# Kernel optimization log

Hardware: AMD Instinct MI355X
Metric: run time of the kernel (lower is better)

Reference implementation:

```python
import jax, jax.numpy as jnp
import numpy as np

NU, NM, E, L = 100000, 20000, 3200000, 1000000
FD, H = 128, 64


def setup_inputs() -> dict:
    key = jax.random.key(0)
    ks = jax.random.split(key, 32)
    s = 0.05
    inp = {
        'movie_x': jax.random.normal(ks[0], (NM, FD), jnp.float32),
        'edge_src_user': jax.random.randint(ks[1], (E,), 0, NU),
        'edge_dst_movie': jax.random.randint(ks[2], (E,), 0, NM),
        'label_user': jax.random.randint(ks[3], (L,), 0, NU),
        'label_movie': jax.random.randint(ks[4], (L,), 0, NM),
        'user_emb': jax.random.normal(ks[5], (NU, H), jnp.float32) * s,
        'proj_w': jax.random.normal(ks[6], (FD, H), jnp.float32) * s,
        'proj_b': jnp.zeros((H,), jnp.float32),
        'dec_w1': jax.random.normal(ks[7], (2 * H, H), jnp.float32) * s,
        'dec_b1': jnp.zeros((H,), jnp.float32),
        'dec_w2': jax.random.normal(ks[8], (H, 1), jnp.float32) * s,
        'dec_b2': jnp.zeros((1,), jnp.float32),
    }
    i = 9
    for layer in ('1', '2'):
        for rel in ('um', 'mu'):
            inp[f'w{layer}_{rel}_l'] = jax.random.normal(ks[i], (H, H), jnp.float32) * s; i += 1
            inp[f'b{layer}_{rel}_l'] = jnp.zeros((H,), jnp.float32)
            inp[f'w{layer}_{rel}_r'] = jax.random.normal(ks[i], (H, H), jnp.float32) * s; i += 1
    return inp


def _sage(x_src, x_dst, e_src, e_dst, n_dst, w_l, b_l, w_r):
    # PyG SAGEConv, aggr='mean': out = lin_l(mean_j x_src[j]) + lin_r(x_dst)
    msg = x_src[e_src]                                      # [E, H] gather
    agg = jax.ops.segment_sum(msg, e_dst, num_segments=n_dst)
    cnt = jax.ops.segment_sum(jnp.ones((e_dst.shape[0],), x_src.dtype), e_dst, num_segments=n_dst)
    agg = agg / jnp.maximum(cnt, 1.0)[:, None]
    return agg @ w_l + b_l + x_dst @ w_r


def reference(movie_x, edge_src_user, edge_dst_movie, label_user, label_movie,
              user_emb, proj_w, proj_b,
              w1_um_l, b1_um_l, w1_um_r, w1_mu_l, b1_mu_l, w1_mu_r,
              w2_um_l, b2_um_l, w2_um_r, w2_mu_l, b2_mu_l, w2_mu_r,
              dec_w1, dec_b1, dec_w2, dec_b2):
    nu, nm = user_emb.shape[0], movie_x.shape[0]
    user0 = user_emb
    movie0 = movie_x @ proj_w + proj_b
    # conv1 (user->movie and movie->user), then ReLU
    movie1 = jax.nn.relu(_sage(user0, movie0, edge_src_user, edge_dst_movie, nm, w1_um_l, b1_um_l, w1_um_r))
    user1 = jax.nn.relu(_sage(movie0, user0, edge_dst_movie, edge_src_user, nu, w1_mu_l, b1_mu_l, w1_mu_r))
    # conv2 (no activation)
    movie2 = _sage(user1, movie1, edge_src_user, edge_dst_movie, nm, w2_um_l, b2_um_l, w2_um_r)
    user2 = _sage(movie1, user1, edge_dst_movie, edge_src_user, nu, w2_mu_l, b2_mu_l, w2_mu_r)
    # edge decoder: gather -> concat -> MLP
    x = jnp.concatenate([user2[label_user], movie2[label_movie]], axis=-1)  # [L, 2H]
    x = jax.nn.relu(x @ dec_w1 + dec_b1)
    return x @ dec_w2 + dec_b2
```

## Files before the change

### kernel.cpp

```cpp
#include <hip/hip_runtime.h>

static constexpr int NU = 100000;
static constexpr int NM = 20000;
static constexpr int NE = 3200000;
static constexpr int NL = 1000000;
static constexpr int FD = 128;
static constexpr int H  = 64;

static constexpr int MBK = 16;
static constexpr int UBK = 64;
static constexpr int NBM = NM / MBK;
static constexpr int NBU = (NU + UBK - 1) / UBK;
static constexpr int NBT = NBM + NBU;
static constexpr int BIN_CHUNK = 16384;
static constexpr int CAP_M = 4096;
static constexpr int CAP_U = 3072;

typedef __attribute__((ext_vector_type(8))) short short8v;
typedef __attribute__((ext_vector_type(4))) float f32x4;

__device__ __forceinline__ ushort bf16rne(float x) {
  unsigned u = __float_as_uint(x);
  return (ushort)((u + 0x7fffu + ((u >> 16) & 1u)) >> 16);
}

__global__ void k_binit2(int* __restrict__ bcur_m, int* __restrict__ bcur_u) {
  int i = blockIdx.x * 256 + threadIdx.x;
  if (i < NBM) bcur_m[i] = i * CAP_M;
  if (i < NBU) bcur_u[i] = i * CAP_U;
}

__global__ void __launch_bounds__(256) k_bin(const int* __restrict__ esrc,
                                             const int* __restrict__ edst,
                                             int* __restrict__ bcur_m,
                                             int* __restrict__ bcur_u,
                                             unsigned* __restrict__ pairs_m,
                                             unsigned* __restrict__ pairs_u) {
  __shared__ int cnt[NBT];
  __shared__ int base[NBT];
  int tid = threadIdx.x;
  for (int i = tid; i < NBT; i += 256) cnt[i] = 0;
  __syncthreads();
  int e0 = blockIdx.x * BIN_CHUNK;
  int e1 = min(e0 + BIN_CHUNK, NE);
  for (int e = e0 + tid; e < e1; e += 256) {
    int s = esrc[e], d = edst[e];
    atomicAdd(&cnt[d >> 4], 1);
    atomicAdd(&cnt[NBM + (s >> 6)], 1);
  }
  __syncthreads();
  for (int i = tid; i < NBT; i += 256) {
    int c = cnt[i];
    if (c > 0)
      base[i] = (i < NBM) ? atomicAdd(&bcur_m[i], c) : atomicAdd(&bcur_u[i - NBM], c);
    cnt[i] = 0;
  }
  __syncthreads();
  for (int e = e0 + tid; e < e1; e += 256) {
    int s = esrc[e], d = edst[e];
    int bm = d >> 4;
    int r = atomicAdd(&cnt[bm], 1);
    pairs_m[base[bm] + r] = ((unsigned)(d & 15) << 17) | (unsigned)s;
    int bu = NBM + (s >> 6);
    int r2 = atomicAdd(&cnt[bu], 1);
    pairs_u[base[bu] + r2] = ((unsigned)(s & 63) << 15) | (unsigned)d;
  }
}

template <int NPB>
__global__ void __launch_bounds__(256) k_sortb3(const unsigned* __restrict__ pairs,
                                                const int* __restrict__ bcur,
                                                int* __restrict__ start,
                                                int* __restrict__ deg,
                                                int* __restrict__ out_idx,
                                                int n, int shift, unsigned mask, int cap) {
  __shared__ int cnt[NPB];
  __shared__ int cbase[NPB];
  int tid = threadIdx.x;
  if (tid < NPB) cnt[tid] = 0;
  __syncthreads();
  int e0 = blockIdx.x * cap;
  int e1 = bcur[blockIdx.x];
  for (int e = e0 + tid; e < e1; e += 256) {
    unsigned v = pairs[e];
    atomicAdd(&cnt[v >> shift], 1);
  }
  __syncthreads();
  if (tid < 64) {
    int c = (tid < NPB) ? cnt[tid] : 0;
    int v = c;
    #pragma unroll
    for (int off = 1; off < NPB; off <<= 1) {
      int t = __shfl_up(v, off, 64);
      if (tid >= off) v += t;
    }
    if (tid < NPB) {
      int node = blockIdx.x * NPB + tid;
      int basee = e0 + v - c;
      cbase[tid] = basee;
      if (node < n) { start[node] = basee; deg[node] = c; }
      cnt[tid] = 0;
    }
  }
  __syncthreads();
  for (int e = e0 + tid; e < e1; e += 256) {
    unsigned v = pairs[e];
    int loc = (int)(v >> shift);
    int r = atomicAdd(&cnt[loc], 1);
    out_idx[cbase[loc] + r] = (int)(v & mask);
  }
}

__global__ void __launch_bounds__(256) k_agg2c(
    int gm,
    const ushort* __restrict__ fM, const int* __restrict__ stM, const int* __restrict__ dgM,
    const int* __restrict__ idxM, float* __restrict__ outM, int nM,
    const ushort* __restrict__ fU, const int* __restrict__ stU, const int* __restrict__ dgU,
    const int* __restrict__ idxU, float* __restrict__ outU, int nU) {
  const ushort* feat; const int* st; const int* dg; const int* idxs; float* out; int n, b;
  if ((int)blockIdx.x < gm) { feat = fM; st = stM; dg = dgM; idxs = idxM; out = outM; n = nM; b = blockIdx.x; }
  else { feat = fU; st = stU; dg = dgU; idxs = idxU; out = outU; n = nU; b = blockIdx.x - gm; }
  int lane = threadIdx.x & 63;
  int f4 = lane & 15, p = lane >> 4;
  int d = b * 4 + (threadIdx.x >> 6);
  if (d >= n) return;
  int s = st[d], degn = dg[d];
  int e = s + degn;
  float a0 = 0.f, a1 = 0.f, a2 = 0.f, a3 = 0.f;
  int i = s;
  for (; i + 16 <= e; i += 16) {
    int s0 = idxs[i + 0 + p];
    int s1 = idxs[i + 4 + p];
    int s2 = idxs[i + 8 + p];
    int s3 = idxs[i + 12 + p];
    uint2 v0 = *(const uint2*)(feat + ((size_t)s0 << 6) + (f4 << 2));
    uint2 v1 = *(const uint2*)(feat + ((size_t)s1 << 6) + (f4 << 2));
    uint2 v2 = *(const uint2*)(feat + ((size_t)s2 << 6) + (f4 << 2));
    uint2 v3 = *(const uint2*)(feat + ((size_t)s3 << 6) + (f4 << 2));
    a0 += __uint_as_float(v0.x << 16); a1 += __uint_as_float(v0.x & 0xffff0000u);
    a2 += __uint_as_float(v0.y << 16); a3 += __uint_as_float(v0.y & 0xffff0000u);
    a0 += __uint_as_float(v1.x << 16); a1 += __uint_as_float(v1.x & 0xffff0000u);
    a2 += __uint_as_float(v1.y << 16); a3 += __uint_as_float(v1.y & 0xffff0000u);
    a0 += __uint_as_float(v2.x << 16); a1 += __uint_as_float(v2.x & 0xffff0000u);
    a2 += __uint_as_float(v2.y << 16); a3 += __uint_as_float(v2.y & 0xffff0000u);
    a0 += __uint_as_float(v3.x << 16); a1 += __uint_as_float(v3.x & 0xffff0000u);
    a2 += __uint_as_float(v3.y << 16); a3 += __uint_as_float(v3.y & 0xffff0000u);
  }
  for (; i < e; i += 4) {
    int ii = i + p;
    bool ok = ii < e;
    int sj = idxs[ok ? ii : i];
    uint2 v = *(const uint2*)(feat + ((size_t)sj << 6) + (f4 << 2));
    if (!ok) { v.x = 0u; v.y = 0u; }
    a0 += __uint_as_float(v.x << 16); a1 += __uint_as_float(v.x & 0xffff0000u);
    a2 += __uint_as_float(v.y << 16); a3 += __uint_as_float(v.y & 0xffff0000u);
  }
  a0 += __shfl_xor(a0, 16, 64); a1 += __shfl_xor(a1, 16, 64);
  a2 += __shfl_xor(a2, 16, 64); a3 += __shfl_xor(a3, 16, 64);
  a0 += __shfl_xor(a0, 32, 64); a1 += __shfl_xor(a1, 32, 64);
  a2 += __shfl_xor(a2, 32, 64); a3 += __shfl_xor(a3, 32, 64);
  if (p == 0) {
    float inv = 1.f / fmaxf((float)degn, 1.f);
    float4 o = make_float4(a0 * inv, a1 * inv, a2 * inv, a3 * inv);
    *(float4*)&out[((size_t)d << 6) + (f4 << 2)] = o;
  }
}

__global__ void __launch_bounds__(256) k_proj16(const float* __restrict__ x,
                                                const float* __restrict__ w,
                                                const float* __restrict__ b,
                                                float* __restrict__ out,
                                                ushort* __restrict__ outh) {
  __shared__ float sw[FD * H];
  __shared__ float sx[16][FD];
  int tid = threadIdx.x;
  int r0 = blockIdx.x * 16;
  #pragma unroll
  for (int it = 0; it < 8; ++it) {
    int idx = tid + it * 256;
    ((float4*)sw)[idx] = ((const float4*)w)[idx];
  }
  #pragma unroll
  for (int it = 0; it < 2; ++it) {
    int idx = tid + it * 256;
    int row = idx >> 5, q = idx & 31;
    *(float4*)&sx[row][q * 4] = ((const float4*)x)[(size_t)(r0 + row) * 32 + q];
  }
  __syncthreads();
  int col = tid & 63, rg = tid >> 6;
  float bb = b[col];
  float acc[4];
  #pragma unroll
  for (int j = 0; j < 4; ++j) acc[j] = bb;
  #pragma unroll 4
  for (int k4 = 0; k4 < 32; ++k4) {
    float w0 = sw[(k4 * 4 + 0) * H + col], w1 = sw[(k4 * 4 + 1) * H + col];
    float w2 = sw[(k4 * 4 + 2) * H + col], w3 = sw[(k4 * 4 + 3) * H + col];
    #pragma unroll
    for (int j = 0; j < 4; ++j) {
      float4 a = *(const float4*)&sx[rg + j * 4][k4 * 4];
      acc[j] += a.x * w0 + a.y * w1 + a.z * w2 + a.w * w3;
    }
  }
  #pragma unroll
  for (int j = 0; j < 4; ++j) {
    size_t o = (size_t)(r0 + rg + j * 4) * H + col;
    out[o] = acc[j];
    outh[o] = bf16rne(acc[j]);
  }
}

__global__ void __launch_bounds__(256) k_sage16(
    int gm,
    const float* __restrict__ aggM, const float* __restrict__ xdM,
    const float* __restrict__ wlM, const float* __restrict__ wrM,
    const float* __restrict__ blM, float* __restrict__ outfM, ushort* __restrict__ outhM,
    const float* __restrict__ aggU, const float* __restrict__ xdU,
    const float* __restrict__ wlU, const float* __restrict__ wrU,
    const float* __restrict__ blU, float* __restrict__ outfU, ushort* __restrict__ outhU,
    int relu) {
  __shared__ float swl[H * H];
  __shared__ float swr[H * H];
  __shared__ float sa[16][H];
  __shared__ float sd[16][H];
  int tid = threadIdx.x;
  const float *agg, *xd, *wl, *wr, *bl; float* outf; ushort* outh; int r0;
  if ((int)blockIdx.x < gm) {
    agg = aggM; xd = xdM; wl = wlM; wr = wrM; bl = blM; outf = outfM; outh = outhM;
    r0 = blockIdx.x * 16;
  } else {
    agg = aggU; xd = xdU; wl = wlU; wr = wrU; bl = blU; outf = outfU; outh = outhU;
    r0 = (blockIdx.x - gm) * 16;
  }
  #pragma unroll
  for (int it = 0; it < 4; ++it) {
    int idx = tid + it * 256;
    ((float4*)swl)[idx] = ((const float4*)wl)[idx];
    ((float4*)swr)[idx] = ((const float4*)wr)[idx];
  }
  {
    int row = tid >> 4, q = tid & 15;
    *(float4*)&sa[row][q * 4] = ((const float4*)agg)[(size_t)(r0 + row) * 16 + q];
    *(float4*)&sd[row][q * 4] = ((const float4*)xd)[(size_t)(r0 + row) * 16 + q];
  }
  __syncthreads();
  int col = tid & 63, rg = tid >> 6;
  float b = bl[col];
  float acc[4];
  #pragma unroll
  for (int j = 0; j < 4; ++j) acc[j] = b;
  #pragma unroll 4
  for (int k4 = 0; k4 < 16; ++k4) {
    float w0 = swl[(k4 * 4 + 0) * H + col], w1 = swl[(k4 * 4 + 1) * H + col];
    float w2 = swl[(k4 * 4 + 2) * H + col], w3 = swl[(k4 * 4 + 3) * H + col];
    float v0 = swr[(k4 * 4 + 0) * H + col], v1 = swr[(k4 * 4 + 1) * H + col];
    float v2 = swr[(k4 * 4 + 2) * H + col], v3 = swr[(k4 * 4 + 3) * H + col];
    #pragma unroll
    for (int j = 0; j < 4; ++j) {
      int r = rg + j * 4;
      float4 a = *(const float4*)&sa[r][k4 * 4];
      float4 d = *(const float4*)&sd[r][k4 * 4];
      acc[j] += a.x * w0 + a.y * w1 + a.z * w2 + a.w * w3;
      acc[j] += d.x * v0 + d.y * v1 + d.z * v2 + d.w * v3;
    }
  }
  #pragma unroll
  for (int j = 0; j < 4; ++j) {
    int r = rg + j * 4;
    float v = relu ? fmaxf(acc[j], 0.f) : acc[j];
    size_t o = (size_t)(r0 + r) * H + col;
    if (outf) outf[o] = v;
    if (outh) outh[o] = bf16rne(v);
  }
}

__global__ void __launch_bounds__(256) k_cvtb(const float* __restrict__ src,
                                              ushort* __restrict__ dst, int n4) {
  int i = blockIdx.x * 256 + threadIdx.x;
  if (i >= n4) return;
  float4 v = ((const float4*)src)[i];
  ushort4 o;
  o.x = bf16rne(v.x); o.y = bf16rne(v.y); o.z = bf16rne(v.z); o.w = bf16rne(v.w);
  ((ushort4*)dst)[i] = o;
}

__global__ void k_packw(const float* __restrict__ w1, ushort* __restrict__ pw) {
  int tid = threadIdx.x;
  for (int it = 0; it < 4; ++it) {
    int q = tid + it * 256;
    int kt = q >> 8, ct = (q >> 6) & 3, l = q & 63;
    int kg = l >> 4, cg = l & 15;
    #pragma unroll
    for (int j = 0; j < 8; ++j) {
      int k = kt * 32 + kg * 8 + j;
      int c = ct * 16 + cg;
      float x = w1[k * 64 + c];
      unsigned u = __float_as_uint(x);
      unsigned r = (u + 0x7fffu + ((u >> 16) & 1u)) >> 16;
      float res = x - __uint_as_float(r << 16);
      pw[q * 8 + j] = (ushort)r;
      pw[8192 + q * 8 + j] = (ushort)(__float_as_uint(res) >> 16);
    }
  }
}

__global__ void __launch_bounds__(256) k_dec_mfma(
    const ushort* __restrict__ uhi, const ushort* __restrict__ mhi,
    const int* __restrict__ lu, const int* __restrict__ lm,
    const ushort* __restrict__ pw,
    const float* __restrict__ b1, const float* __restrict__ w2,
    const float* __restrict__ b2, float* __restrict__ out) {
  __shared__ ushort sB[2 * 16 * 64 * 8];
  int tid = threadIdx.x;
  #pragma unroll
  for (int it = 0; it < 8; ++it) {
    int idx = tid + it * 256;
    ((float4*)sB)[idx] = ((const float4*)pw)[idx];
  }
  __syncthreads();
  int l = tid & 63, w = tid >> 6;
  int cg = l & 15, kg = l >> 4;
  float w2f[4], b1f[4];
  #pragma unroll
  for (int ct = 0; ct < 4; ++ct) {
    w2f[ct] = w2[ct * 16 + cg];
    b1f[ct] = b1[ct * 16 + cg];
  }
  float b2v = b2[0];
  for (int t = 0; t < 4; ++t) {
    int Lb = blockIdx.x * 256 + w * 64 + t * 16;
    int lab = min(Lb + cg, NL - 1);
    int nu = lu[lab], nm = lm[lab];
    const size_t ub = (size_t)nu * 64 + kg * 8;
    const size_t mb = (size_t)nm * 64 + kg * 8;
    short8v ah[4];
    ah[0] = *(const short8v*)(uhi + ub);
    ah[1] = *(const short8v*)(uhi + ub + 32);
    ah[2] = *(const short8v*)(mhi + mb);
    ah[3] = *(const short8v*)(mhi + mb + 32);
    f32x4 acc[4];
    #pragma unroll
    for (int ct = 0; ct < 4; ++ct) acc[ct] = (f32x4){b1f[ct], b1f[ct], b1f[ct], b1f[ct]};
    #pragma unroll
    for (int kt = 0; kt < 4; ++kt) {
      #pragma unroll
      for (int ct = 0; ct < 4; ++ct) {
        const int f = kt * 4 + ct;
        short8v bh = *(const short8v*)&sB[(size_t)(f * 64 + l) * 8];
        short8v bl_ = *(const short8v*)&sB[(size_t)((16 + f) * 64 + l) * 8];
        acc[ct] = __builtin_amdgcn_mfma_f32_16x16x32_bf16(ah[kt], bh, acc[ct], 0, 0, 0);
        acc[ct] = __builtin_amdgcn_mfma_f32_16x16x32_bf16(ah[kt], bl_, acc[ct], 0, 0, 0);
      }
    }
    float p[4];
    #pragma unroll
    for (int r = 0; r < 4; ++r) {
      p[r] = fmaxf(acc[0][r], 0.f) * w2f[0] + fmaxf(acc[1][r], 0.f) * w2f[1] +
             fmaxf(acc[2][r], 0.f) * w2f[2] + fmaxf(acc[3][r], 0.f) * w2f[3];
    }
    #pragma unroll
    for (int m = 8; m >= 1; m >>= 1) {
      #pragma unroll
      for (int r = 0; r < 4; ++r) p[r] += __shfl_xor(p[r], m, 64);
    }
    if (cg == 0) {
      #pragma unroll
      for (int r = 0; r < 4; ++r) {
        int row = Lb + kg * 4 + r;
        if (row < NL) out[row] = p[r] + b2v;
      }
    }
  }
}

extern "C" void kernel_launch(void* const* d_in, const int* in_sizes, int n_in,
                              void* d_out, int out_size, void* d_ws, size_t ws_size,
                              hipStream_t stream) {
  const float* movie_x  = (const float*)d_in[0];
  const int*   esrc     = (const int*)d_in[1];
  const int*   edst     = (const int*)d_in[2];
  const int*   lu       = (const int*)d_in[3];
  const int*   lm       = (const int*)d_in[4];
  const float* user_emb = (const float*)d_in[5];
  const float* proj_w   = (const float*)d_in[6];
  const float* proj_b   = (const float*)d_in[7];
  const float* dec_w1   = (const float*)d_in[8];
  const float* dec_b1   = (const float*)d_in[9];
  const float* dec_w2   = (const float*)d_in[10];
  const float* dec_b2   = (const float*)d_in[11];
  const float* w1_um_l  = (const float*)d_in[12];
  const float* b1_um_l  = (const float*)d_in[13];
  const float* w1_um_r  = (const float*)d_in[14];
  const float* w1_mu_l  = (const float*)d_in[15];
  const float* b1_mu_l  = (const float*)d_in[16];
  const float* w1_mu_r  = (const float*)d_in[17];
  const float* w2_um_l  = (const float*)d_in[18];
  const float* b2_um_l  = (const float*)d_in[19];
  const float* w2_um_r  = (const float*)d_in[20];
  const float* w2_mu_l  = (const float*)d_in[21];
  const float* b2_mu_l  = (const float*)d_in[22];
  const float* w2_mu_r  = (const float*)d_in[23];

  char* ws = (char*)d_ws;
  size_t off = 0;
  auto alloc = [&](size_t bytes) {
    void* p = ws + off;
    off = (off + bytes + 255) & ~(size_t)255;
    return p;
  };
  float* movie0   = (float*)alloc((size_t)NM * H * 4);
  float* movie1   = (float*)alloc((size_t)NM * H * 4);
  float* user1    = (float*)alloc((size_t)NU * H * 4);
  float* agg_m    = (float*)alloc((size_t)NM * H * 4);
  float* agg_u    = (float*)alloc((size_t)NU * H * 4);
  unsigned* pairs_m = (unsigned*)user1;
  unsigned* pairs_u = pairs_m + (size_t)NBM * CAP_M;
  ushort* uembh   = (ushort*)alloc((size_t)NU * H * 2);
  ushort* movie0h = (ushort*)alloc((size_t)NM * H * 2);
  ushort* movie1h = (ushort*)alloc((size_t)NM * H * 2);
  ushort* user1h  = (ushort*)alloc((size_t)NU * H * 2);
  ushort* uhi     = (ushort*)alloc((size_t)NU * H * 2);
  ushort* mhi     = (ushort*)alloc((size_t)NM * H * 2);
  int* st_m      = (int*)alloc((size_t)NM * 4);
  int* st_u      = (int*)alloc((size_t)NU * 4);
  int* dg_m      = (int*)alloc((size_t)NM * 4);
  int* dg_u      = (int*)alloc((size_t)NU * 4);
  int* bcur_m    = (int*)alloc((size_t)NBM * 4);
  int* bcur_u    = (int*)alloc((size_t)NBU * 4);
  int* su_by_m   = (int*)alloc((size_t)NBM * CAP_M * 4);
  int* sm_by_u   = (int*)alloc((size_t)NBU * CAP_U * 4);
  ushort* pw     = (ushort*)alloc((size_t)2 * 16 * 64 * 8 * 2);
  (void)ws_size; (void)in_sizes; (void)n_in; (void)out_size;

  k_binit2<<<(NBU + 255) / 256, 256, 0, stream>>>(bcur_m, bcur_u);
  int bblocks = (NE + BIN_CHUNK - 1) / BIN_CHUNK;
  k_bin<<<bblocks, 256, 0, stream>>>(esrc, edst, bcur_m, bcur_u, pairs_m, pairs_u);
  k_sortb3<MBK><<<NBM, 256, 0, stream>>>(pairs_m, bcur_m, st_m, dg_m, su_by_m, NM, 17, 0x1FFFFu, CAP_M);
  k_sortb3<UBK><<<NBU, 256, 0, stream>>>(pairs_u, bcur_u, st_u, dg_u, sm_by_u, NU, 15, 0x7FFFu, CAP_U);

  k_proj16<<<NM / 16, 256, 0, stream>>>(movie_x, proj_w, proj_b, movie0, movie0h);
  k_cvtb<<<(NU * H / 4 + 255) / 256, 256, 0, stream>>>(user_emb, uembh, NU * H / 4);
  k_packw<<<1, 256, 0, stream>>>(dec_w1, pw);

  const int GAM = NM / 4, GAU = NU / 4;
  const int GSM = NM / 16, GSU = NU / 16;

  k_agg2c<<<GAM + GAU, 256, 0, stream>>>(GAM,
      uembh,   st_m, dg_m, su_by_m, agg_m, NM,
      movie0h, st_u, dg_u, sm_by_u, agg_u, NU);
  k_sage16<<<GSM + GSU, 256, 0, stream>>>(GSM,
      agg_m, movie0,   w1_um_l, w1_um_r, b1_um_l, movie1, movie1h,
      agg_u, user_emb, w1_mu_l, w1_mu_r, b1_mu_l, user1,  user1h, 1);

  k_agg2c<<<GAM + GAU, 256, 0, stream>>>(GAM,
      user1h,  st_m, dg_m, su_by_m, agg_m, NM,
      movie1h, st_u, dg_u, sm_by_u, agg_u, NU);
  k_sage16<<<GSM + GSU, 256, 0, stream>>>(GSM,
      agg_m, movie1, w2_um_l, w2_um_r, b2_um_l, (float*)nullptr, mhi,
      agg_u, user1,  w2_mu_l, w2_mu_r, b2_mu_l, (float*)nullptr, uhi, 0);

  k_dec_mfma<<<(NL + 255) / 256, 256, 0, stream>>>(uhi, mhi, lu, lm, pw,
                                                   dec_b1, dec_w2, dec_b2, (float*)d_out);
}
```

Measured before the change: 513.8 us.

## Split edge binning per side with LDS staging for coalesced scatter; merge sort kernels

The combined binning kernel is replaced by per-side binning blocks. Each block first counts edges per bucket, computes local offsets with a block scan, and stages packed pairs in LDS ordered by bucket, then writes them to global memory in contiguous runs per bucket rather than scattering them. The two per-side bucket sort launches are merged into one launch with runtime parameters. The intent is to cut scattered global writes and launch overhead. In exchange, edges are read twice across the two sides, LDS use rises to about 40KB per block, and the bucket-offset setup in each block adds serial work.

```diff
diff --git a/kernel.cpp b/kernel.cpp
--- a/kernel.cpp
+++ b/kernel.cpp
@@ -11,10 +11,9 @@
 static constexpr int UBK = 64;
 static constexpr int NBM = NM / MBK;
 static constexpr int NBU = (NU + UBK - 1) / UBK;
-static constexpr int NBT = NBM + NBU;
-static constexpr int BIN_CHUNK = 16384;
 static constexpr int CAP_M = 4096;
 static constexpr int CAP_U = 3072;
+static constexpr int B2C = 8192;
 
 typedef __attribute__((ext_vector_type(8))) short short8v;
 typedef __attribute__((ext_vector_type(4))) float f32x4;
@@ -30,77 +29,110 @@
   if (i < NBU) bcur_u[i] = i * CAP_U;
 }
 
-__global__ void __launch_bounds__(256) k_bin(const int* __restrict__ esrc,
-                                             const int* __restrict__ edst,
-                                             int* __restrict__ bcur_m,
-                                             int* __restrict__ bcur_u,
-                                             unsigned* __restrict__ pairs_m,
-                                             unsigned* __restrict__ pairs_u) {
-  __shared__ int cnt[NBT];
-  __shared__ int base[NBT];
-  int tid = threadIdx.x;
-  for (int i = tid; i < NBT; i += 256) cnt[i] = 0;
-  __syncthreads();
-  int e0 = blockIdx.x * BIN_CHUNK;
-  int e1 = min(e0 + BIN_CHUNK, NE);
+__global__ void __launch_bounds__(256) k_bin2(
+    const int* __restrict__ esrc, const int* __restrict__ edst,
+    int* __restrict__ bcur_m, int* __restrict__ bcur_u,
+    unsigned* __restrict__ pairs_m, unsigned* __restrict__ pairs_u, int nbPerSide) {
+  __shared__ unsigned stage[B2C];
+  __shared__ int cnt[NBU];
+  __shared__ int lofs[NBU];
+  __shared__ int gbase[NBU];
+  __shared__ int wpart[4];
+  int tid = threadIdx.x;
+  bool um = (int)blockIdx.x < nbPerSide;
+  int cb = um ? blockIdx.x : blockIdx.x - nbPerSide;
+  int nbs = um ? NBM : NBU;
+  int* bcur = um ? bcur_m : bcur_u;
+  unsigned* pairs = um ? pairs_m : pairs_u;
+  int e0 = cb * B2C, e1 = min(e0 + B2C, NE);
+  for (int i = tid; i < nbs; i += 256) cnt[i] = 0;
+  __syncthreads();
+  for (int e = e0 + tid; e < e1; e += 256) {
+    int key = um ? edst[e] : esrc[e];
+    int b = um ? (key >> 4) : (key >> 6);
+    atomicAdd(&cnt[b], 1);
+  }
+  __syncthreads();
+  int PT = (nbs + 255) / 256;
+  int lo = tid * PT, hi = min(lo + PT, nbs);
+  int run = 0;
+  for (int i = lo; i < hi; ++i) { lofs[i] = run; run += cnt[i]; }
+  int part = run;
+  int lane = tid & 63, wid = tid >> 6;
+  int v = part;
+  #pragma unroll
+  for (int off = 1; off < 64; off <<= 1) {
+    int t = __shfl_up(v, off, 64);
+    if (lane >= off) v += t;
+  }
+  if (lane == 63) wpart[wid] = v;
+  __syncthreads();
+  int woff = 0;
+  for (int wj = 0; wj < wid; ++wj) woff += wpart[wj];
+  int excl = woff + v - part;
+  for (int i = lo; i < hi; ++i) {
+    lofs[i] += excl;
+    int c = cnt[i];
+    gbase[i] = (c > 0) ? atomicAdd(&bcur[i], c) : 0;
+    cnt[i] = 0;
+  }
+  __syncthreads();
   for (int e = e0 + tid; e < e1; e += 256) {
     int s = esrc[e], d = edst[e];
-    atomicAdd(&cnt[d >> 4], 1);
-    atomicAdd(&cnt[NBM + (s >> 6)], 1);
-  }
-  __syncthreads();
-  for (int i = tid; i < NBT; i += 256) {
-    int c = cnt[i];
-    if (c > 0)
-      base[i] = (i < NBM) ? atomicAdd(&bcur_m[i], c) : atomicAdd(&bcur_u[i - NBM], c);
-    cnt[i] = 0;
-  }
-  __syncthreads();
-  for (int e = e0 + tid; e < e1; e += 256) {
-    int s = esrc[e], d = edst[e];
-    int bm = d >> 4;
-    int r = atomicAdd(&cnt[bm], 1);
-    pairs_m[base[bm] + r] = ((unsigned)(d & 15) << 17) | (unsigned)s;
-    int bu = NBM + (s >> 6);
-    int r2 = atomicAdd(&cnt[bu], 1);
-    pairs_u[base[bu] + r2] = ((unsigned)(s & 63) << 15) | (unsigned)d;
-  }
-}
-
-template <int NPB>
-__global__ void __launch_bounds__(256) k_sortb3(const unsigned* __restrict__ pairs,
-                                                const int* __restrict__ bcur,
-                                                int* __restrict__ start,
-                                                int* __restrict__ deg,
-                                                int* __restrict__ out_idx,
-                                                int n, int shift, unsigned mask, int cap) {
-  __shared__ int cnt[NPB];
-  __shared__ int cbase[NPB];
-  int tid = threadIdx.x;
-  if (tid < NPB) cnt[tid] = 0;
-  __syncthreads();
-  int e0 = blockIdx.x * cap;
-  int e1 = bcur[blockIdx.x];
-  for (int e = e0 + tid; e < e1; e += 256) {
-    unsigned v = pairs[e];
-    atomicAdd(&cnt[v >> shift], 1);
-  }
+    if (um) {
+      int b = d >> 4;
+      int r = atomicAdd(&cnt[b], 1);
+      stage[lofs[b] + r] = ((unsigned)d << 17) | (unsigned)s;
+    } else {
+      int b = s >> 6;
+      int r = atomicAdd(&cnt[b], 1);
+      stage[lofs[b] + r] = ((unsigned)s << 15) | (unsigned)d;
+    }
+  }
+  __syncthreads();
+  int ne = e1 - e0;
+  for (int slot = tid; slot < ne; slot += 256) {
+    unsigned v2 = stage[slot];
+    int b = um ? ((int)(v2 >> 17) >> 4) : ((int)(v2 >> 15) >> 6);
+    pairs[gbase[b] + (slot - lofs[b])] = v2 & 0x1FFFFFu;
+  }
+}
+
+__global__ void __launch_bounds__(256) k_sortb4(
+    const unsigned* __restrict__ pairs_m, const unsigned* __restrict__ pairs_u,
+    const int* __restrict__ bcur_m, const int* __restrict__ bcur_u,
+    int* __restrict__ st_m, int* __restrict__ dg_m, int* __restrict__ out_m,
+    int* __restrict__ st_u, int* __restrict__ dg_u, int* __restrict__ out_u) {
+  __shared__ int cnt[64];
+  __shared__ int cbase[64];
+  const unsigned* pairs; const int* bcur; int* start; int* deg; int* out_idx;
+  int b, npb, shift, cap, n; unsigned mask;
+  if ((int)blockIdx.x < NBM) {
+    pairs = pairs_m; bcur = bcur_m; start = st_m; deg = dg_m; out_idx = out_m;
+    b = blockIdx.x; npb = MBK; shift = 17; mask = 0x1FFFFu; cap = CAP_M; n = NM;
+  } else {
+    pairs = pairs_u; bcur = bcur_u; start = st_u; deg = dg_u; out_idx = out_u;
+    b = blockIdx.x - NBM; npb = UBK; shift = 15; mask = 0x7FFFu; cap = CAP_U; n = NU;
+  }
+  int tid = threadIdx.x;
+  if (tid < 64) cnt[tid] = 0;
+  __syncthreads();
+  int e0 = b * cap, e1 = bcur[b];
+  for (int e = e0 + tid; e < e1; e += 256) atomicAdd(&cnt[pairs[e] >> shift], 1);
   __syncthreads();
   if (tid < 64) {
-    int c = (tid < NPB) ? cnt[tid] : 0;
+    int c = cnt[tid];
     int v = c;
     #pragma unroll
-    for (int off = 1; off < NPB; off <<= 1) {
+    for (int off = 1; off < 64; off <<= 1) {
       int t = __shfl_up(v, off, 64);
       if (tid >= off) v += t;
     }
-    if (tid < NPB) {
-      int node = blockIdx.x * NPB + tid;
-      int basee = e0 + v - c;
-      cbase[tid] = basee;
-      if (node < n) { start[node] = basee; deg[node] = c; }
-      cnt[tid] = 0;
-    }
+    int basee = e0 + v - c;
+    cbase[tid] = basee;
+    int node = b * npb + tid;
+    if (tid < npb && node < n) { start[node] = basee; deg[node] = c; }
+    cnt[tid] = 0;
   }
   __syncthreads();
   for (int e = e0 + tid; e < e1; e += 256) {
@@ -433,10 +465,11 @@
   (void)ws_size; (void)in_sizes; (void)n_in; (void)out_size;
 
   k_binit2<<<(NBU + 255) / 256, 256, 0, stream>>>(bcur_m, bcur_u);
-  int bblocks = (NE + BIN_CHUNK - 1) / BIN_CHUNK;
-  k_bin<<<bblocks, 256, 0, stream>>>(esrc, edst, bcur_m, bcur_u, pairs_m, pairs_u);
-  k_sortb3<MBK><<<NBM, 256, 0, stream>>>(pairs_m, bcur_m, st_m, dg_m, su_by_m, NM, 17, 0x1FFFFu, CAP_M);
-  k_sortb3<UBK><<<NBU, 256, 0, stream>>>(pairs_u, bcur_u, st_u, dg_u, sm_by_u, NU, 15, 0x7FFFu, CAP_U);
+  int nbPerSide = (NE + B2C - 1) / B2C;
+  k_bin2<<<2 * nbPerSide, 256, 0, stream>>>(esrc, edst, bcur_m, bcur_u,
+                                            pairs_m, pairs_u, nbPerSide);
+  k_sortb4<<<NBM + NBU, 256, 0, stream>>>(pairs_m, pairs_u, bcur_m, bcur_u,
+                                          st_m, dg_m, su_by_m, st_u, dg_u, sm_by_u);
 
   k_proj16<<<NM / 16, 256, 0, stream>>>(movie_x, proj_w, proj_b, movie0, movie0h);
   k_cvtb<<<(NU * H / 4 + 255) / 256, 256, 0, stream>>>(user_emb, uembh, NU * H / 4);
```

New measurement: 520.1 us. About the same (+1.2%).
